# Kernel tuning notes

Hardware: AMD Instinct MI355X
Metric: run time of the kernel (lower is better)

The kernel has to match this reference:

```python
import jax, jax.numpy as jnp
import numpy as np

B, S, E = 4, 2048, 1024


def setup_inputs() -> dict:
    key = jax.random.key(0)
    ks = jax.random.split(key, 7)
    s = 1.0 / np.sqrt(E)  # torch Linear default init scale (uniform bound)
    inp = {
        "input": jax.random.normal(ks[0], (B, S, E), dtype=jnp.float32),
        "masked": 1,
        "W_q": jax.random.uniform(ks[1], (E, E), jnp.float32, -s, s),
        "b_q": jax.random.uniform(ks[2], (E,), jnp.float32, -s, s),
        "W_k": jax.random.uniform(ks[3], (E, E), jnp.float32, -s, s),
        "b_k": jax.random.uniform(ks[4], (E,), jnp.float32, -s, s),
        "W_v": jax.random.uniform(ks[5], (E, E), jnp.float32, -s, s),
        "b_v": jax.random.uniform(ks[6], (E,), jnp.float32, -s, s),
    }
    return inp


def reference(input, masked, W_q, b_q, W_k, b_k, W_v, b_v):
    # torch.nn.Linear: y = x @ W.T + b
    q = jnp.einsum("bse,fe->bsf", input, W_q) + b_q
    k = jnp.einsum("bse,fe->bsf", input, W_k) + b_k
    v = jnp.einsum("bse,fe->bsf", input, W_v) + b_v
    d = q.shape[-1]
    scores = jnp.einsum("bqd,bkd->bqk", q, k) / jnp.sqrt(jnp.float32(d))
    if masked:
        Sq = scores.shape[1]
        causal = jnp.tril(jnp.ones((Sq, Sq), dtype=bool))  # [S,S], broadcast over batch
        scores = jnp.where(causal, scores, -jnp.inf)
    attn = jax.nn.softmax(scores, axis=-1)
    return jnp.einsum("bqk,bkd->bqd", attn, v)
```

## Files before the change

### kernel.cpp

```cpp
#include <hip/hip_runtime.h>

typedef _Float16 f16;
typedef f16 f16x8 __attribute__((ext_vector_type(8)));
typedef f16 f16x4v __attribute__((ext_vector_type(4)));
typedef float f32x4 __attribute__((ext_vector_type(4)));

__device__ __forceinline__ void async_ld16(const void* g, void* l) {
    __builtin_amdgcn_global_load_lds(
        (const __attribute__((address_space(1))) unsigned int*)g,
        (__attribute__((address_space(3))) unsigned int*)l, 16, 0, 0);
}

#define VMC(n) asm volatile("s_waitcnt vmcnt(" #n ")" ::: "memory")
#define BAR __builtin_amdgcn_s_barrier()

#define STG(b, op, kh, P, P1, tOff) do {                                        \
    char* d_ = (char*)smem + (b) * 65536 + (op) * 32768 + (kh) * 16384 + stgBase; \
    async_ld16((P)  + (tOff) * 64 + (kh) * 32, d_);                             \
    async_ld16((P1) + (tOff) * 64 + (kh) * 32, d_ + 8192);                      \
} while (0)
#define RD_A(b, kk) do {                                                        \
    const char* s_ = (const char*)smem + (b) * 65536 + (kk) * 16384 + aOff;     \
    _Pragma("unroll") for (int m_ = 0; m_ < 8; ++m_)                            \
        af[m_] = *(const f16x8*)(s_ + m_ * 1024);                               \
} while (0)
#define RD_B2(b, kk, n0_) do {                                                  \
    const char* s_ = (const char*)smem + (b) * 65536 + 32768 + (kk) * 16384 + bOff; \
    bf[(n0_)]     = *(const f16x8*)(s_ + ((n0_)) * 1024);                       \
    bf[(n0_) + 1] = *(const f16x8*)(s_ + ((n0_) + 1) * 1024);                   \
} while (0)
#define FENCE_MM(n0_) do {                                                      \
    __builtin_amdgcn_s_barrier();                                               \
    asm volatile("s_waitcnt lgkmcnt(0)" ::: "memory");                          \
    __builtin_amdgcn_sched_barrier(0);                                          \
    __builtin_amdgcn_s_setprio(1);                                              \
    _Pragma("unroll") for (int m_ = 0; m_ < 8; ++m_) {                          \
        acc[m_][(n0_)]     = __builtin_amdgcn_mfma_f32_16x16x32_f16(af[m_], bf[(n0_)],     acc[m_][(n0_)],     0, 0, 0); \
        acc[m_][(n0_) + 1] = __builtin_amdgcn_mfma_f32_16x16x32_f16(af[m_], bf[(n0_) + 1], acc[m_][(n0_) + 1], 0, 0, 0); \
    }                                                                           \
    __builtin_amdgcn_s_setprio(0);                                              \
} while (0)

__global__ __launch_bounds__(512, 2) void scores256(
    const f16* __restrict__ Q, const f16* __restrict__ K,
    f16* __restrict__ P, float* __restrict__ rowsum,
    const int* __restrict__ maskedp)
{
    const int masked = *maskedp;
    const int bx = blockIdx.x, by = blockIdx.y, bz = blockIdx.z;
    if (masked && bx > by) return;
    const int mBase = by * 256, nBase = bx * 256;

    __shared__ __align__(16) f16 smem[65536];
    const int tid = threadIdx.x;
    const int wave = tid >> 6, lane = tid & 63;
    const int wrow = wave >> 2, wcol = wave & 3;
    const int quad = lane >> 4, l16 = lane & 15;
    const int rowLane = tid >> 2;
    const int cOff = ((tid & 3) ^ ((tid >> 3) & 3)) * 8;
    const int stgBase = wave * 1024;
    const int swz  = (quad ^ ((l16 >> 1) & 3)) * 16;
    const int aOff = (wrow * 128 + l16) * 64 + swz;
    const int bOff = (wcol * 64 + l16) * 64 + swz;
    f32x4 acc[8][4];
#pragma unroll
    for (int m = 0; m < 8; ++m)
#pragma unroll
        for (int n = 0; n < 4; ++n) acc[m][n] = (f32x4){0.f, 0.f, 0.f, 0.f};
    f16x8 af[8], bf[4];

    const f16* Ab  = Q + (long)bz * (2048L * 1024);
    const f16* Btb = K + (long)bz * (2048L * 1024);
    const f16* pA  = Ab  + (long)(mBase + rowLane) * 1024 + cOff;
    const f16* pA1 = pA + 128 * 1024;
    const f16* pB  = Btb + (long)(nBase + rowLane) * 1024 + cOff;
    const f16* pB1 = pB + 128 * 1024;

    STG(0, 0, 0, pA, pA1, 0); STG(0, 1, 0, pB, pB1, 0);
    STG(0, 0, 1, pA, pA1, 0); STG(0, 1, 1, pB, pB1, 0);
    STG(1, 0, 0, pA, pA1, 1); STG(1, 1, 0, pB, pB1, 1);
    VMC(4);
    BAR;

#pragma unroll 1
    for (int i = 0; i < 7; ++i) {
        RD_A(0, 0); RD_B2(0, 0, 0); STG(1, 0, 1, pA, pA1, 1);
        FENCE_MM(0); BAR;
        RD_B2(0, 0, 2);             STG(1, 1, 1, pB, pB1, 1);
        FENCE_MM(2); BAR;
        RD_A(0, 1); RD_B2(0, 1, 0); STG(0, 0, 0, pA, pA1, 2);
        FENCE_MM(0); BAR;
        RD_B2(0, 1, 2);             STG(0, 1, 0, pB, pB1, 2);
        FENCE_MM(2); VMC(4); BAR;
        RD_A(1, 0); RD_B2(1, 0, 0); STG(0, 0, 1, pA, pA1, 2);
        FENCE_MM(0); BAR;
        RD_B2(1, 0, 2);             STG(0, 1, 1, pB, pB1, 2);
        FENCE_MM(2); BAR;
        RD_A(1, 1); RD_B2(1, 1, 0); STG(1, 0, 0, pA, pA1, 3);
        FENCE_MM(0); BAR;
        RD_B2(1, 1, 2);             STG(1, 1, 0, pB, pB1, 3);
        FENCE_MM(2); VMC(4); BAR;
        pA += 128; pA1 += 128; pB += 128; pB1 += 128;
    }
    RD_A(0, 0); RD_B2(0, 0, 0); STG(1, 0, 1, pA, pA1, 1);
    FENCE_MM(0); BAR;
    RD_B2(0, 0, 2);             STG(1, 1, 1, pB, pB1, 1);
    FENCE_MM(2); BAR;
    RD_A(0, 1); RD_B2(0, 1, 0);
    FENCE_MM(0); BAR;
    RD_B2(0, 1, 2);
    FENCE_MM(2); VMC(0); BAR;
    RD_A(1, 0); RD_B2(1, 0, 0);
    FENCE_MM(0); BAR;
    RD_B2(1, 0, 2);
    FENCE_MM(2); BAR;
    RD_A(1, 1); RD_B2(1, 1, 0);
    FENCE_MM(0); BAR;
    RD_B2(1, 1, 2);
    FENCE_MM(2);

    f16* Crow = P + (long)bz * (2048L * 2048);
    float* rsb = rowsum + bz * 2048;
#pragma unroll
    for (int m = 0; m < 8; ++m) {
        float rs[4] = {0.f, 0.f, 0.f, 0.f};
#pragma unroll
        for (int n = 0; n < 4; ++n)
#pragma unroll
            for (int r = 0; r < 4; ++r) {
                const int row = mBase + wrow * 128 + m * 16 + quad * 4 + r;
                const int col = nBase + wcol * 64 + n * 16 + l16;
                float e = __expf(acc[m][n][r] * 0.03125f);
                if (masked && col > row) e = 0.f;
                const f16 hv = (f16)e;
                Crow[(long)row * 2048 + col] = hv;
                rs[r] += (float)hv;
            }
#pragma unroll
        for (int r = 0; r < 4; ++r) {
            float s = rs[r];
            s += __shfl_xor(s, 1);
            s += __shfl_xor(s, 2);
            s += __shfl_xor(s, 4);
            s += __shfl_xor(s, 8);
            if (l16 == 0) {
                const int row = mBase + wrow * 128 + m * 16 + quad * 4 + r;
                atomicAdd(&rsb[row], s);
            }
        }
    }
}

#undef STG
#undef RD_A
#undef RD_B2
#undef FENCE_MM

#define QSTG_A(b, kh, tOff) do {                                                \
    char* d_ = (char*)smem + (b) * 49152 + (kh) * 8192 + stgBase;               \
    async_ld16(pA + (tOff) * 64 + (kh) * 32, d_);                               \
} while (0)
#define QSTG_B(b, kh, tOff) do {                                                \
    char* d_ = (char*)smem + (b) * 49152 + 16384 + (kh) * 16384 + stgBase;      \
    async_ld16(pB  + (tOff) * 64 + (kh) * 32, d_);                              \
    async_ld16(pB1 + (tOff) * 64 + (kh) * 32, d_ + 8192);                       \
} while (0)
#define QRD(b, kk) do {                                                         \
    const char* sa_ = (const char*)smem + (b) * 49152 + (kk) * 8192 + aOff;     \
    _Pragma("unroll") for (int m_ = 0; m_ < 4; ++m_)                            \
        af[m_] = *(const f16x8*)(sa_ + m_ * 1024);                              \
    const char* sb_ = (const char*)smem + (b) * 49152 + 16384 + (kk) * 16384 + bOff; \
    _Pragma("unroll") for (int n_ = 0; n_ < 4; ++n_)                            \
        bf[n_] = *(const f16x8*)(sb_ + n_ * 1024);                              \
} while (0)
#define QFENCE do {                                                             \
    __builtin_amdgcn_s_barrier();                                               \
    asm volatile("s_waitcnt lgkmcnt(0)" ::: "memory");                          \
    __builtin_amdgcn_sched_barrier(0);                                          \
    __builtin_amdgcn_s_setprio(1);                                              \
    _Pragma("unroll") for (int m_ = 0; m_ < 4; ++m_)                            \
        _Pragma("unroll") for (int n_ = 0; n_ < 4; ++n_)                        \
            acc[m_][n_] = __builtin_amdgcn_mfma_f32_16x16x32_f16(af[m_], bf[n_], acc[m_][n_], 0, 0, 0); \
    __builtin_amdgcn_s_setprio(0);                                              \
} while (0)

__global__ __launch_bounds__(512, 2) void qkv128(
    const f16* __restrict__ A, const f16* __restrict__ Bt,
    const float* __restrict__ b_q, const float* __restrict__ b_k,
    const float* __restrict__ b_v,
    f16* __restrict__ Q16, f16* __restrict__ K16, f16* __restrict__ Vt16)
{
    int bid = blockIdx.x;
    bid = (bid & 7) * 96 + (bid >> 3);
    const int by = bid / 12, bx = bid - by * 12;
    const int mBase = by * 128, nBase = bx * 256;

    __shared__ __align__(16) f16 smem[49152];
    const int tid = threadIdx.x;
    const int wave = tid >> 6, lane = tid & 63;
    const int wrow = wave >> 2, wcol = wave & 3;
    const int quad = lane >> 4, l16 = lane & 15;
    const int rowLane = tid >> 2;
    const int cOff = ((tid & 3) ^ ((tid >> 3) & 3)) * 8;
    const int stgBase = wave * 1024;
    const int swz  = (quad ^ ((l16 >> 1) & 3)) * 16;
    const int aOff = (wrow * 64 + l16) * 64 + swz;
    const int bOff = (wcol * 64 + l16) * 64 + swz;

    const f16* pA  = A  + (long)(mBase + rowLane) * 1024 + cOff;
    const f16* pB  = Bt + (long)(nBase + rowLane) * 1024 + cOff;
    const f16* pB1 = pB + 128 * 1024;

    f32x4 acc[4][4];
#pragma unroll
    for (int m = 0; m < 4; ++m)
#pragma unroll
        for (int n = 0; n < 4; ++n) acc[m][n] = (f32x4){0.f, 0.f, 0.f, 0.f};
    f16x8 af[4], bf[4];

    QSTG_A(0, 0, 0); QSTG_B(0, 0, 0);
    QSTG_A(0, 1, 0); QSTG_B(0, 1, 0);
    QSTG_A(1, 0, 1); QSTG_B(1, 0, 1);
    VMC(3);
    BAR;

#pragma unroll 1
    for (int i = 0; i < 7; ++i) {
        QRD(0, 0); QSTG_A(1, 1, 1); QSTG_B(1, 1, 1);
        QFENCE; VMC(6); BAR;
        QRD(0, 1); QSTG_A(0, 0, 2); QSTG_B(0, 0, 2);
        QFENCE; VMC(6); BAR;
        QRD(1, 0); QSTG_A(0, 1, 2); QSTG_B(0, 1, 2);
        QFENCE; VMC(6); BAR;
        QRD(1, 1); QSTG_A(1, 0, 3); QSTG_B(1, 0, 3);
        QFENCE; VMC(6); BAR;
        pA += 128; pB += 128; pB1 += 128;
    }
    QRD(0, 0); QSTG_A(1, 1, 1); QSTG_B(1, 1, 1);
    QFENCE; VMC(6); BAR;
    QRD(0, 1);
    QFENCE; VMC(3); BAR;
    QRD(1, 0);
    QFENCE; VMC(0); BAR;
    QRD(1, 1);
    QFENCE;
    BAR;

    const int seg = nBase >> 10;
    const float* bs = (seg == 0) ? b_q : (seg == 1) ? b_k : b_v;
    const int lcb = (nBase & 1023) + wcol * 64;
    float bvv[4];
#pragma unroll
    for (int n = 0; n < 4; ++n) bvv[n] = bs[lcb + n * 16 + l16];

    if (seg < 2) {
        f16* dst = (seg == 0) ? Q16 : K16;
#pragma unroll
        for (int m = 0; m < 4; ++m)
#pragma unroll
            for (int n = 0; n < 4; ++n)
#pragma unroll
                for (int r = 0; r < 4; ++r) {
                    const int row = mBase + wrow * 64 + m * 16 + quad * 4 + r;
                    dst[(long)row * 1024 + lcb + n * 16 + l16] =
                        (f16)(acc[m][n][r] + bvv[n]);
                }
    } else {
        const int b = mBase >> 11;
        const int s0 = (mBase & 2047) + wrow * 64;
        const int e0 = (nBase & 1023) + wcol * 64;
        f16* epiW = smem + wave * (64 * 72);
#pragma unroll
        for (int m = 0; m < 4; ++m)
#pragma unroll
            for (int n = 0; n < 4; ++n) {
                f16x4v pk;
#pragma unroll
                for (int r = 0; r < 4; ++r)
                    pk[r] = (f16)(acc[m][n][r] + bvv[n]);
                *(f16x4v*)&epiW[(n * 16 + l16) * 72 + m * 16 + quad * 4] = pk;
            }
        asm volatile("s_waitcnt lgkmcnt(0)" ::: "memory");
#pragma unroll
        for (int it = 0; it < 8; ++it) {
            const int e = it * 8 + (lane >> 3);
            const f16x8 v = *(const f16x8*)&epiW[e * 72 + (lane & 7) * 8];
            *(f16x8*)(Vt16 + ((long)b * 1024 + e0 + e) * 2048 + s0 +
                      (lane & 7) * 8) = v;
        }
    }
}

#undef QSTG_A
#undef QSTG_B
#undef QRD
#undef QFENCE

#define PSTG_A(b, kh, tOff) do {                                                \
    char* d_ = (char*)smem + (b) * 32768 + (kh) * 8192 + stgBase;               \
    async_ld16(pA  + (tOff) * 64 + (kh) * 32, d_);                              \
    async_ld16(pA1 + (tOff) * 64 + (kh) * 32, d_ + 4096);                       \
} while (0)
#define PSTG_B(b, kh, tOff) do {                                                \
    char* d_ = (char*)smem + (b) * 32768 + 16384 + (kh) * 8192 + stgBase;       \
    async_ld16(pB  + (tOff) * 64 + (kh) * 32, d_);                              \
    async_ld16(pB1 + (tOff) * 64 + (kh) * 32, d_ + 4096);                       \
} while (0)
#define PRD(b, kk) do {                                                         \
    const char* sa_ = (const char*)smem + (b) * 32768 + (kk) * 8192 + aOff;     \
    _Pragma("unroll") for (int m_ = 0; m_ < 4; ++m_)                            \
        af[m_] = *(const f16x8*)(sa_ + m_ * 1024);                              \
    const char* sb_ = (const char*)smem + (b) * 32768 + 16384 + (kk) * 8192 + bOff; \
    _Pragma("unroll") for (int n_ = 0; n_ < 4; ++n_)                            \
        bf[n_] = *(const f16x8*)(sb_ + n_ * 1024);                              \
} while (0)
#define PFENCE do {                                                             \
    __builtin_amdgcn_s_barrier();                                               \
    asm volatile("s_waitcnt lgkmcnt(0)" ::: "memory");                          \
    __builtin_amdgcn_sched_barrier(0);                                          \
    __builtin_amdgcn_s_setprio(1);                                              \
    _Pragma("unroll") for (int m_ = 0; m_ < 4; ++m_)                            \
        _Pragma("unroll") for (int n_ = 0; n_ < 4; ++n_)                        \
            acc[m_][n_] = __builtin_amdgcn_mfma_f32_16x16x32_f16(af[m_], bf[n_], acc[m_][n_], 0, 0, 0); \
    __builtin_amdgcn_s_setprio(0);                                              \
} while (0)

__global__ __launch_bounds__(256, 2) void pv128(
    const f16* __restrict__ P, const f16* __restrict__ Vt,
    const float* __restrict__ rowsum, float* __restrict__ out,
    const int* __restrict__ maskedp)
{
    const int masked = *maskedp;
    const int bx = blockIdx.x, bz = blockIdx.z;
    const int by = gridDim.y - 1 - blockIdx.y;
    const int mBase = by * 128, nBase = bx * 128;
    const int nIter = masked ? ((by >> 1) + 1) * 2 : 16;

    __shared__ __align__(16) f16 smem[32768];
    const int tid = threadIdx.x;
    const int wave = tid >> 6, lane = tid & 63;
    const int wrow = wave >> 1, wcol = wave & 1;
    const int quad = lane >> 4, l16 = lane & 15;
    const int rowLane = tid >> 2;
    const int cOff = ((tid & 3) ^ ((tid >> 3) & 3)) * 8;
    const int stgBase = wave * 1024;
    const int swz  = (quad ^ ((l16 >> 1) & 3)) * 16;
    const int aOff = (wrow * 64 + l16) * 64 + swz;
    const int bOff = (wcol * 64 + l16) * 64 + swz;

    const f16* Pb = P  + (long)bz * (2048L * 2048);
    const f16* Vb = Vt + (long)bz * (1024L * 2048);
    const f16* pA  = Pb + (long)(mBase + rowLane) * 2048 + cOff;
    const f16* pA1 = pA + 64 * 2048;
    const f16* pB  = Vb + (long)(nBase + rowLane) * 2048 + cOff;
    const f16* pB1 = pB + 64 * 2048;

    f32x4 acc[4][4];
#pragma unroll
    for (int m = 0; m < 4; ++m)
#pragma unroll
        for (int n = 0; n < 4; ++n) acc[m][n] = (f32x4){0.f, 0.f, 0.f, 0.f};
    f16x8 af[4], bf[4];

    PSTG_A(0, 0, 0); PSTG_B(0, 0, 0);
    PSTG_A(0, 1, 0); PSTG_B(0, 1, 0);
    PSTG_A(1, 0, 1); PSTG_B(1, 0, 1);
    VMC(4);
    BAR;

#pragma unroll 1
    for (int i = 0; i < nIter - 1; ++i) {
        PRD(0, 0); PSTG_A(1, 1, 1); PSTG_B(1, 1, 1);
        PFENCE; VMC(8); BAR;
        PRD(0, 1); PSTG_A(0, 0, 2); PSTG_B(0, 0, 2);
        PFENCE; VMC(8); BAR;
        PRD(1, 0); PSTG_A(0, 1, 2); PSTG_B(0, 1, 2);
        PFENCE; VMC(8); BAR;
        PRD(1, 1); PSTG_A(1, 0, 3); PSTG_B(1, 0, 3);
        PFENCE; VMC(8); BAR;
        pA += 128; pA1 += 128; pB += 128; pB1 += 128;
    }
    PRD(0, 0); PSTG_A(1, 1, 1); PSTG_B(1, 1, 1);
    PFENCE; VMC(8); BAR;
    PRD(0, 1);
    PFENCE; VMC(4); BAR;
    PRD(1, 0);
    PFENCE; VMC(0); BAR;
    PRD(1, 1);
    PFENCE;

    const float* rsb = rowsum + bz * 2048;
    float* ob = out + (long)bz * (2048L * 1024);
#pragma unroll
    for (int m = 0; m < 4; ++m)
#pragma unroll
        for (int r = 0; r < 4; ++r) {
            const int row = mBase + wrow * 64 + m * 16 + quad * 4 + r;
            const float inv = 1.f / rsb[row];
#pragma unroll
            for (int n = 0; n < 4; ++n) {
                const int col = nBase + wcol * 64 + n * 16 + l16;
                ob[(long)row * 1024 + col] = acc[m][n][r] * inv;
            }
        }
}

#undef PSTG_A
#undef PSTG_B
#undef PRD
#undef PFENCE
#undef VMC
#undef BAR

__global__ void cvt_inp(const float* __restrict__ in, f16* __restrict__ out, int n4)
{
    const int i = blockIdx.x * blockDim.x + threadIdx.x;
    if (i >= n4) return;
    const float4 v = ((const float4*)in)[i];
    f16x4v o;
    o[0] = (f16)v.x; o[1] = (f16)v.y; o[2] = (f16)v.z; o[3] = (f16)v.w;
    ((f16x4v*)out)[i] = o;
}

__global__ void cvt_w3(const float* __restrict__ W0, const float* __restrict__ W1,
                       const float* __restrict__ W2, f16* __restrict__ out)
{
    const int bxx = blockIdx.x;
    const int which = bxx >> 10;
    const float* src = (which == 0) ? W0 : (which == 1) ? W1 : W2;
    const int i = (bxx & 1023) * 256 + threadIdx.x;
    const float4 v = ((const float4*)src)[i];
    f16x4v o;
    o[0] = (f16)v.x; o[1] = (f16)v.y; o[2] = (f16)v.z; o[3] = (f16)v.w;
    ((f16x4v*)(out + (long)which * 1024 * 1024))[i] = o;
}

extern "C" void kernel_launch(void* const* d_in, const int* in_sizes, int n_in,
                              void* d_out, int out_size, void* d_ws, size_t ws_size,
                              hipStream_t stream)
{
    const float* inp = (const float*)d_in[0];
    const int* masked = (const int*)d_in[1];
    const float* Wq = (const float*)d_in[2];
    const float* bq = (const float*)d_in[3];
    const float* Wk = (const float*)d_in[4];
    const float* bk = (const float*)d_in[5];
    const float* Wv = (const float*)d_in[6];
    const float* bv = (const float*)d_in[7];
    float* out = (float*)d_out;

    const int Bb = 4, S = 2048, E = 1024;
    const long nTok = (long)Bb * S;

    char* ws = (char*)d_ws;
    f16* inp16 = (f16*)ws;   ws += nTok * E * 2;
    f16* W3    = (f16*)ws;   ws += (long)3 * E * E * 2;
    f16* Q16   = (f16*)ws;   ws += nTok * E * 2;
    f16* K16   = (f16*)ws;   ws += nTok * E * 2;
    f16* Vt16  = (f16*)ws;   ws += nTok * E * 2;
    f16* P16   = (f16*)ws;   ws += (long)Bb * S * S * 2;
    float* rsum = (float*)ws; ws += nTok * 4;

    dim3 blk(256);

    hipMemsetAsync(rsum, 0, nTok * 4, stream);
    cvt_inp<<<(int)(nTok * E / 4 / 256), blk, 0, stream>>>(inp, inp16, (int)(nTok * E / 4));
    cvt_w3<<<3 * 1024, blk, 0, stream>>>(Wq, Wk, Wv, W3);

    qkv128<<<dim3(768), dim3(512), 0, stream>>>(
        inp16, W3, bq, bk, bv, Q16, K16, Vt16);

    scores256<<<dim3(8, 8, 4), dim3(512), 0, stream>>>(
        Q16, K16, P16, rsum, masked);

    pv128<<<dim3(8, 16, 4), dim3(256), 0, stream>>>(
        P16, Vt16, rsum, out, masked);
}
```

Baseline: 252.8 us.

## Compute softmax row sums inside PV kernel and merge conversion kernels

Drops the per-row atomicAdd reduction and the rowsum buffer from the scores kernel. The PV kernel now accumulates row sums from the P fragments it already loads, using fdot2 against ones, then reduces them with cross-lane shuffles. The two fp32-to-fp16 conversion kernels are merged into one launch and the memset is removed. This saves atomics, a memset and a launch, at the cost of extra ALU work in the PV inner loop.

Measured after the change: 241.2 us. 1.05x faster.

```diff
diff --git a/kernel.cpp b/kernel.cpp
--- a/kernel.cpp
+++ b/kernel.cpp
@@ -3,6 +3,7 @@
 typedef _Float16 f16;
 typedef f16 f16x8 __attribute__((ext_vector_type(8)));
 typedef f16 f16x4v __attribute__((ext_vector_type(4)));
+typedef f16 f16x2v __attribute__((ext_vector_type(2)));
 typedef float f32x4 __attribute__((ext_vector_type(4)));
 
 __device__ __forceinline__ void async_ld16(const void* g, void* l) {
@@ -13,6 +14,7 @@
 
 #define VMC(n) asm volatile("s_waitcnt vmcnt(" #n ")" ::: "memory")
 #define BAR __builtin_amdgcn_s_barrier()
+
 
 #define STG(b, op, kh, P, P1, tOff) do {                                        \
     char* d_ = (char*)smem + (b) * 65536 + (op) * 32768 + (kh) * 16384 + stgBase; \
@@ -43,8 +45,7 @@
 
 __global__ __launch_bounds__(512, 2) void scores256(
     const f16* __restrict__ Q, const f16* __restrict__ K,
-    f16* __restrict__ P, float* __restrict__ rowsum,
-    const int* __restrict__ maskedp)
+    f16* __restrict__ P, const int* __restrict__ maskedp)
 {
     const int masked = *maskedp;
     const int bx = blockIdx.x, by = blockIdx.y, bz = blockIdx.z;
@@ -120,10 +121,8 @@
     FENCE_MM(2);
 
     f16* Crow = P + (long)bz * (2048L * 2048);
-    float* rsb = rowsum + bz * 2048;
-#pragma unroll
-    for (int m = 0; m < 8; ++m) {
-        float rs[4] = {0.f, 0.f, 0.f, 0.f};
+#pragma unroll
+    for (int m = 0; m < 8; ++m)
 #pragma unroll
         for (int n = 0; n < 4; ++n)
 #pragma unroll
@@ -132,23 +131,8 @@
                 const int col = nBase + wcol * 64 + n * 16 + l16;
                 float e = __expf(acc[m][n][r] * 0.03125f);
                 if (masked && col > row) e = 0.f;
-                const f16 hv = (f16)e;
-                Crow[(long)row * 2048 + col] = hv;
-                rs[r] += (float)hv;
+                Crow[(long)row * 2048 + col] = (f16)e;
             }
-#pragma unroll
-        for (int r = 0; r < 4; ++r) {
-            float s = rs[r];
-            s += __shfl_xor(s, 1);
-            s += __shfl_xor(s, 2);
-            s += __shfl_xor(s, 4);
-            s += __shfl_xor(s, 8);
-            if (l16 == 0) {
-                const int row = mBase + wrow * 128 + m * 16 + quad * 4 + r;
-                atomicAdd(&rsb[row], s);
-            }
-        }
-    }
 }
 
 #undef STG
@@ -296,6 +280,29 @@
 #undef QRD
 #undef QFENCE
 
+#if defined(__has_builtin)
+#if __has_builtin(__builtin_amdgcn_fdot2)
+#define HAVE_FDOT2 1
+#endif
+#endif
+
+#ifdef HAVE_FDOT2
+#define PSUM do {                                                               \
+    const f16x2v one_ = {(f16)1, (f16)1};                                       \
+    _Pragma("unroll") for (int m_ = 0; m_ < 4; ++m_) {                          \
+        const f16x2v* ph_ = (const f16x2v*)&af[m_];                             \
+        _Pragma("unroll") for (int j_ = 0; j_ < 4; ++j_)                        \
+            rs[m_] = __builtin_amdgcn_fdot2(ph_[j_], one_, rs[m_], false);      \
+    }                                                                           \
+} while (0)
+#else
+#define PSUM do {                                                               \
+    _Pragma("unroll") for (int m_ = 0; m_ < 4; ++m_)                            \
+        _Pragma("unroll") for (int j_ = 0; j_ < 8; ++j_)                        \
+            rs[m_] += (float)af[m_][j_];                                        \
+} while (0)
+#endif
+
 #define PSTG_A(b, kh, tOff) do {                                                \
     char* d_ = (char*)smem + (b) * 32768 + (kh) * 8192 + stgBase;               \
     async_ld16(pA  + (tOff) * 64 + (kh) * 32, d_);                              \
@@ -323,12 +330,12 @@
         _Pragma("unroll") for (int n_ = 0; n_ < 4; ++n_)                        \
             acc[m_][n_] = __builtin_amdgcn_mfma_f32_16x16x32_f16(af[m_], bf[n_], acc[m_][n_], 0, 0, 0); \
     __builtin_amdgcn_s_setprio(0);                                              \
+    PSUM;                                                                       \
 } while (0)
 
 __global__ __launch_bounds__(256, 2) void pv128(
     const f16* __restrict__ P, const f16* __restrict__ Vt,
-    const float* __restrict__ rowsum, float* __restrict__ out,
-    const int* __restrict__ maskedp)
+    float* __restrict__ out, const int* __restrict__ maskedp)
 {
     const int masked = *maskedp;
     const int bx = blockIdx.x, bz = blockIdx.z;
@@ -361,6 +368,7 @@
 #pragma unroll
         for (int n = 0; n < 4; ++n) acc[m][n] = (f32x4){0.f, 0.f, 0.f, 0.f};
     f16x8 af[4], bf[4];
+    float rs[4] = {0.f, 0.f, 0.f, 0.f};
 
     PSTG_A(0, 0, 0); PSTG_B(0, 0, 0);
     PSTG_A(0, 1, 0); PSTG_B(0, 1, 0);
@@ -389,14 +397,19 @@
     PRD(1, 1);
     PFENCE;
 
-    const float* rsb = rowsum + bz * 2048;
+#pragma unroll
+    for (int m = 0; m < 4; ++m) {
+        rs[m] += __shfl_xor(rs[m], 16);
+        rs[m] += __shfl_xor(rs[m], 32);
+    }
+
     float* ob = out + (long)bz * (2048L * 1024);
 #pragma unroll
     for (int m = 0; m < 4; ++m)
 #pragma unroll
         for (int r = 0; r < 4; ++r) {
             const int row = mBase + wrow * 64 + m * 16 + quad * 4 + r;
-            const float inv = 1.f / rsb[row];
+            const float inv = 1.f / __shfl(rs[m], quad * 4 + r);
 #pragma unroll
             for (int n = 0; n < 4; ++n) {
                 const int col = nBase + wcol * 64 + n * 16 + l16;
@@ -409,30 +422,34 @@
 #undef PSTG_B
 #undef PRD
 #undef PFENCE
+#undef PSUM
 #undef VMC
 #undef BAR
 
-__global__ void cvt_inp(const float* __restrict__ in, f16* __restrict__ out, int n4)
-{
-    const int i = blockIdx.x * blockDim.x + threadIdx.x;
-    if (i >= n4) return;
-    const float4 v = ((const float4*)in)[i];
-    f16x4v o;
-    o[0] = (f16)v.x; o[1] = (f16)v.y; o[2] = (f16)v.z; o[3] = (f16)v.w;
-    ((f16x4v*)out)[i] = o;
-}
-
-__global__ void cvt_w3(const float* __restrict__ W0, const float* __restrict__ W1,
-                       const float* __restrict__ W2, f16* __restrict__ out)
+__global__ void cvt_all(const float* __restrict__ inp,
+                        const float* __restrict__ W0,
+                        const float* __restrict__ W1,
+                        const float* __restrict__ W2,
+                        f16* __restrict__ inp16, f16* __restrict__ W3)
 {
     const int bxx = blockIdx.x;
-    const int which = bxx >> 10;
-    const float* src = (which == 0) ? W0 : (which == 1) ? W1 : W2;
-    const int i = (bxx & 1023) * 256 + threadIdx.x;
+    const float* src;
+    f16* dst;
+    int i;
+    if (bxx < 8192) {
+        src = inp; dst = inp16;
+        i = bxx * 256 + threadIdx.x;
+    } else {
+        const int wb = bxx - 8192;
+        const int which = wb >> 10;
+        src = (which == 0) ? W0 : (which == 1) ? W1 : W2;
+        dst = W3 + (long)which * 1024 * 1024;
+        i = (wb & 1023) * 256 + threadIdx.x;
+    }
     const float4 v = ((const float4*)src)[i];
     f16x4v o;
     o[0] = (f16)v.x; o[1] = (f16)v.y; o[2] = (f16)v.z; o[3] = (f16)v.w;
-    ((f16x4v*)(out + (long)which * 1024 * 1024))[i] = o;
+    ((f16x4v*)dst)[i] = o;
 }
 
 extern "C" void kernel_launch(void* const* d_in, const int* in_sizes, int n_in,
@@ -449,8 +466,8 @@
     const float* bv = (const float*)d_in[7];
     float* out = (float*)d_out;
 
-    const int Bb = 4, S = 2048, E = 1024;
-    const long nTok = (long)Bb * S;
+    const int S = 2048, E = 1024;
+    const long nTok = (long)4 * S;
 
     char* ws = (char*)d_ws;
     f16* inp16 = (f16*)ws;   ws += nTok * E * 2;
@@ -458,21 +475,17 @@
     f16* Q16   = (f16*)ws;   ws += nTok * E * 2;
     f16* K16   = (f16*)ws;   ws += nTok * E * 2;
     f16* Vt16  = (f16*)ws;   ws += nTok * E * 2;
-    f16* P16   = (f16*)ws;   ws += (long)Bb * S * S * 2;
-    float* rsum = (float*)ws; ws += nTok * 4;
-
-    dim3 blk(256);
-
-    hipMemsetAsync(rsum, 0, nTok * 4, stream);
-    cvt_inp<<<(int)(nTok * E / 4 / 256), blk, 0, stream>>>(inp, inp16, (int)(nTok * E / 4));
-    cvt_w3<<<3 * 1024, blk, 0, stream>>>(Wq, Wk, Wv, W3);
+    f16* P16   = (f16*)ws;   ws += (long)4 * S * S * 2;
+
+    cvt_all<<<dim3(8192 + 3072), dim3(256), 0, stream>>>(
+        inp, Wq, Wk, Wv, inp16, W3);
 
     qkv128<<<dim3(768), dim3(512), 0, stream>>>(
         inp16, W3, bq, bk, bv, Q16, K16, Vt16);
 
     scores256<<<dim3(8, 8, 4), dim3(512), 0, stream>>>(
-        Q16, K16, P16, rsum, masked);
+        Q16, K16, P16, masked);
 
     pv128<<<dim3(8, 16, 4), dim3(256), 0, stream>>>(
-        P16, Vt16, rsum, out, masked);
-}
+        P16, Vt16, out, masked);
+}
```
